# Kernel tuning notes

Measured on AMD Instinct MI355X. Metric: run time of the kernel, lower is better.

Reference implementation:

```python
import jax, jax.numpy as jnp
import numpy as np

DIM = 768
HEADS = 12
HEAD_DIM = DIM // HEADS  # 64
GRID = 48               # H = W = 48 tokens
RANK = 8                # LoRA rank


def setup_inputs() -> dict:
    key = jax.random.key(0)
    ks = jax.random.split(key, 20)
    s = 0.02
    inp = {
        "x": jax.random.normal(ks[0], (1, GRID, GRID, DIM), dtype=jnp.float32),
        "Wq": jax.random.normal(ks[1], (DIM, DIM), dtype=jnp.float32) * s,
        "bq": jax.random.normal(ks[2], (DIM,), dtype=jnp.float32) * s,
        "Wk": jax.random.normal(ks[3], (DIM, DIM), dtype=jnp.float32) * s,
        "bk": jax.random.normal(ks[4], (DIM,), dtype=jnp.float32) * s,
        "Wv": jax.random.normal(ks[5], (DIM, DIM), dtype=jnp.float32) * s,
        "bv": jax.random.normal(ks[6], (DIM,), dtype=jnp.float32) * s,
        "Wp": jax.random.normal(ks[7], (DIM, DIM), dtype=jnp.float32) * s,
        "bp": jax.random.normal(ks[8], (DIM,), dtype=jnp.float32) * s,
        "rel_pos_h": jax.random.normal(ks[9], (2 * GRID - 1, HEAD_DIM), dtype=jnp.float32) * s,
        "rel_pos_w": jax.random.normal(ks[10], (2 * GRID - 1, HEAD_DIM), dtype=jnp.float32) * s,
        "Aq": jax.random.normal(ks[11], (DIM, RANK), dtype=jnp.float32) * s,
        "Bq": jax.random.normal(ks[12], (RANK, DIM), dtype=jnp.float32) * s,
        "Ak": jax.random.normal(ks[13], (DIM, RANK), dtype=jnp.float32) * s,
        "Bk": jax.random.normal(ks[14], (RANK, DIM), dtype=jnp.float32) * s,
        "Av": jax.random.normal(ks[15], (DIM, RANK), dtype=jnp.float32) * s,
        "Bv": jax.random.normal(ks[16], (RANK, DIM), dtype=jnp.float32) * s,
    }
    return inp


def _get_rel_pos(size, rel_pos):
    # q_size == k_size == size, rel_pos has exactly 2*size-1 rows -> direct lookup
    idx = jnp.arange(size)[:, None] - jnp.arange(size)[None, :] + (size - 1)
    return rel_pos[idx]  # (size, size, head_dim)


def reference(x, Wq, bq, Wk, bk, Wv, bv, Wp, bp, rel_pos_h, rel_pos_w,
              Aq, Bq, Ak, Bk, Av, Bv):
    B, H, W, _ = x.shape
    N = H * W
    scale = HEAD_DIM ** -0.5

    # QKV projections + LoRA additions
    q = x @ Wq + bq + (x @ Aq) @ Bq
    k = x @ Wk + bk + (x @ Ak) @ Bk
    v = x @ Wv + bv + (x @ Av) @ Bv

    # (B, heads, N, head_dim)
    q = q.reshape(B, N, HEADS, HEAD_DIM).transpose(0, 2, 1, 3)
    k = k.reshape(B, N, HEADS, HEAD_DIM).transpose(0, 2, 1, 3)
    v = v.reshape(B, N, HEADS, HEAD_DIM).transpose(0, 2, 1, 3)

    attn = jnp.einsum('bhnc,bhmc->bhnm', q, k) * scale  # (B, heads, N, N)

    # Decomposed relative position bias (SAM add_decomposed_rel_pos)
    Rh = _get_rel_pos(H, rel_pos_h)  # (H, H, c)
    Rw = _get_rel_pos(W, rel_pos_w)  # (W, W, c)
    r_q = q.reshape(B, HEADS, H, W, HEAD_DIM)
    rel_h = jnp.einsum('bnhwc,hkc->bnhwk', r_q, Rh)  # (B, heads, H, W, H)
    rel_w = jnp.einsum('bnhwc,wkc->bnhwk', r_q, Rw)  # (B, heads, H, W, W)
    attn = (attn.reshape(B, HEADS, H, W, H, W)
            + rel_h[..., :, None] + rel_w[..., None, :]).reshape(B, HEADS, N, N)

    attn = jax.nn.softmax(attn, axis=-1)
    out = jnp.einsum('bhnm,bhmc->bhnc', attn, v)        # (B, heads, N, c)
    out = out.transpose(0, 2, 1, 3).reshape(B, H, W, DIM)
    return out @ Wp + bp
```

## Files before the change

kernel.cpp:

```cpp
#include <hip/hip_runtime.h>


#define DIM   768
#define HEADS 12
#define HD    64
#define NTOK  2304
#define RANK  8
#define GRD   48
#define CHUNKS 3
#define KEYS_PER_CHUNK 768
#define KT_PER 12
#define LOG2E 1.44269504088896f

typedef __attribute__((ext_vector_type(8))) short bf16x8;
typedef __attribute__((ext_vector_type(4))) float f32x4;
typedef unsigned short ushort_t;

__device__ __forceinline__ unsigned short f2bf(float x) {
    union { float f; unsigned u; } v; v.f = x;
    unsigned r = v.u + 0x7fffu + ((v.u >> 16) & 1u);
    return (unsigned short)(r >> 16);
}
__device__ __forceinline__ float bf2f(unsigned short h) {
    return __uint_as_float(((unsigned)h) << 16);
}
__device__ __forceinline__ void gload_lds16(const ushort_t* g, ushort_t* l) {
    __builtin_amdgcn_global_load_lds(
        (const __attribute__((address_space(1))) unsigned int*)g,
        (__attribute__((address_space(3))) unsigned int*)l, 16, 0, 0);
}

__global__ __launch_bounds__(256) void k_prep(
    const float* __restrict__ x, ushort_t* __restrict__ xb,
    const float* __restrict__ rph, const float* __restrict__ rpw,
    ushort_t* __restrict__ rphb, ushort_t* __restrict__ rpwb,
    const float* __restrict__ Wq, const float* __restrict__ Wk,
    const float* __restrict__ Wv, const float* __restrict__ Wp,
    const float* __restrict__ Aq, const float* __restrict__ Bq,
    const float* __restrict__ Ak, const float* __restrict__ Bk,
    const float* __restrict__ Av, const float* __restrict__ Bv,
    ushort_t* __restrict__ WT) {
    int bid = blockIdx.x, tid = threadIdx.x;

    if (bid < 1740) {
        if (bid < 1728) {
            int idx = (bid * 256 + tid) * 4;
            float4 v = *(const float4*)(x + idx);
            ushort4 o = make_ushort4(f2bf(v.x), f2bf(v.y), f2bf(v.z), f2bf(v.w));
            *(ushort4*)(xb + idx) = o;
        } else {
            int e = ((bid - 1728) * 256 + tid) * 4;
            const int TSZ = (2 * GRD - 1) * HD;
            if (e < TSZ) {
                float4 v = *(const float4*)(rph + e);
                ushort4 o = make_ushort4(f2bf(v.x), f2bf(v.y), f2bf(v.z), f2bf(v.w));
                *(ushort4*)(rphb + e) = o;
            } else if (e < 2 * TSZ) {
                float4 v = *(const float4*)(rpw + e - TSZ);
                ushort4 o = make_ushort4(f2bf(v.x), f2bf(v.y), f2bf(v.z), f2bf(v.w));
                *(ushort4*)(rpwb + e - TSZ) = o;
            }
        }
    }

    int kb = (bid % 24) * 32;
    int nb = (bid / 24) * 32;
    int sel = nb / DIM, nmod = nb % DIM;
    const float* W = (sel == 0) ? Wq : (sel == 1) ? Wk : (sel == 2) ? Wv : Wp;
    const float* A = (sel == 0) ? Aq : (sel == 1) ? Ak : Av;
    const float* B = (sel == 0) ? Bq : (sel == 1) ? Bk : Bv;
    __shared__ float T[32][33];
    for (int i = tid; i < 1024; i += 256) {
        int kl = i >> 5, nl = i & 31;
        float v = W[(kb + kl) * DIM + nmod + nl];
        if (sel < 3) {
            #pragma unroll
            for (int r = 0; r < RANK; r++)
                v += A[(kb + kl) * RANK + r] * B[r * DIM + nmod + nl];
        }
        T[kl][nl] = v;
    }
    __syncthreads();
    if (tid < 128) {
        int nl = tid >> 2, k8 = (tid & 3) * 8;
        ushort_t tmp[8];
        #pragma unroll
        for (int q = 0; q < 8; q++) tmp[q] = f2bf(T[k8 + q][nl]);
        *(uint4*)&WT[(size_t)(nb + nl) * DIM + kb + k8] = *(const uint4*)tmp;
    }
}

__global__ __launch_bounds__(256) void k_gemm_qkv(
    const ushort_t* __restrict__ xb, const ushort_t* __restrict__ WT,
    const float* __restrict__ bq, const float* __restrict__ bk,
    const float* __restrict__ bv,
    ushort_t* __restrict__ Qb, ushort_t* __restrict__ Kb,
    ushort_t* __restrict__ Vtb) {
    __shared__ __align__(16) ushort_t As[2][2][128 * 32];
    __shared__ __align__(16) ushort_t Bs[2][2][64 * 32];
    int tid = threadIdx.x;
    int wave = tid >> 6, lane = tid & 63, quad = lane >> 4, l16 = lane & 15;
    int wx = wave & 1, wy = wave >> 1;
    int nb = blockIdx.x * 64, mb = blockIdx.y * 128;

    f32x4 zero = {0.f, 0.f, 0.f, 0.f};
    f32x4 acc[4][2];
    #pragma unroll
    for (int i = 0; i < 4; i++)
        #pragma unroll
        for (int j = 0; j < 2; j++) acc[i][j] = zero;

    int rl = lane >> 2;
    int cl = (lane & 3) * 8;
    const ushort_t* gA = xb + (size_t)(mb + wave * 32 + rl) * DIM + cl;
    const ushort_t* gB = WT + (size_t)(nb + wave * 16 + rl) * DIM + cl;

    auto stage = [&](int k0, int b) {
        gload_lds16(gA + k0,                 &As[b][0][(wave * 32) * 32]);
        gload_lds16(gA + k0 + 16 * DIM,      &As[b][0][(wave * 32) * 32] + 16 * 32);
        gload_lds16(gA + k0 + 32,            &As[b][1][(wave * 32) * 32]);
        gload_lds16(gA + k0 + 32 + 16 * DIM, &As[b][1][(wave * 32) * 32] + 16 * 32);
        gload_lds16(gB + k0,                 &Bs[b][0][(wave * 16) * 32]);
        gload_lds16(gB + k0 + 32,            &Bs[b][1][(wave * 16) * 32]);
    };

    stage(0, 0);
    for (int it = 0; it < 12; ++it) {
        int cur = it & 1;
        if (it < 11) {
            stage((it + 1) * 64, cur ^ 1);
            asm volatile("s_waitcnt vmcnt(6)" ::: "memory");
        } else {
            asm volatile("s_waitcnt vmcnt(0)" ::: "memory");
        }
        __builtin_amdgcn_s_barrier();
        #pragma unroll
        for (int p = 0; p < 2; p++) {
            bf16x8 af[4], bf[2];
            #pragma unroll
            for (int i = 0; i < 4; i++)
                af[i] = *(const bf16x8*)&As[cur][p][(wy * 64 + i * 16 + l16) * 32 + quad * 8];
            #pragma unroll
            for (int j = 0; j < 2; j++)
                bf[j] = *(const bf16x8*)&Bs[cur][p][(wx * 32 + j * 16 + l16) * 32 + quad * 8];
            #pragma unroll
            for (int i = 0; i < 4; i++)
                #pragma unroll
                for (int j = 0; j < 2; j++)
                    acc[i][j] = __builtin_amdgcn_mfma_f32_16x16x32_bf16(af[i], bf[j], acc[i][j], 0, 0, 0);
        }
        __builtin_amdgcn_s_barrier();
    }

    ushort_t* pool = &As[0][0][0];
    int sel = nb / DIM;
    int rem0 = nb - sel * DIM;
    int hh = rem0 >> 6;
    const float* bias = (sel == 0) ? bq : (sel == 1) ? bk : bv;

    __syncthreads();

    if (sel < 2) {
        const int P = 72;
        #pragma unroll
        for (int j = 0; j < 2; j++) {
            int c = wx * 32 + j * 16 + l16;
            float bval = bias[rem0 + c];
            #pragma unroll
            for (int i = 0; i < 4; i++)
                #pragma unroll
                for (int r = 0; r < 4; r++) {
                    int row = wy * 64 + i * 16 + quad * 4 + r;
                    pool[row * P + c] = f2bf(acc[i][j][r] + bval);
                }
        }
        __syncthreads();
        ushort_t* qout = ((sel == 0) ? Qb : Kb) + (size_t)(hh * NTOK + mb) * HD;
        for (int idx = tid; idx < 128 * 8; idx += 256) {
            int row = idx >> 3, s8 = idx & 7;
            uint4 v = *(const uint4*)&pool[row * P + s8 * 8];
            *(uint4*)&qout[(size_t)row * HD + s8 * 8] = v;
        }
    } else {
        const int PV = 136;
        #pragma unroll
        for (int j = 0; j < 2; j++) {
            int c = wx * 32 + j * 16 + l16;
            float bval = bias[rem0 + c];
            #pragma unroll
            for (int i = 0; i < 4; i++)
                #pragma unroll
                for (int r = 0; r < 4; r++) {
                    int row = wy * 64 + i * 16 + quad * 4 + r;
                    pool[c * PV + row] = f2bf(acc[i][j][r] + bval);
                }
        }
        __syncthreads();
        ushort_t* vout = Vtb + (size_t)(hh * HD) * NTOK + mb;
        for (int idx = tid; idx < 64 * 16; idx += 256) {
            int cc = idx >> 4, r8 = idx & 15;
            uint4 v = *(const uint4*)&pool[cc * PV + r8 * 8];
            *(uint4*)&vout[(size_t)cc * NTOK + r8 * 8] = v;
        }
    }
}

__global__ __launch_bounds__(256) void k_relmm(
    const ushort_t* __restrict__ Qb, const ushort_t* __restrict__ rphb,
    const ushort_t* __restrict__ rpwb, float* __restrict__ relH,
    ushort_t* __restrict__ relWb) {
    int id = blockIdx.x * 4 + (threadIdx.x >> 6);
    int lane = threadIdx.x & 63, quad = lane >> 4, l16 = lane & 15;
    bool isW = id >= 1728;
    int t = isW ? id - 1728 : id;
    int ms = t % 3;
    int g  = (t / 3) % GRD;
    int h  = t / (3 * GRD);
    const ushort_t* tab = isW ? rpwb : rphb;

    f32x4 zero = {0.f, 0.f, 0.f, 0.f};
    f32x4 acc[3];
    #pragma unroll
    for (int ct = 0; ct < 3; ct++) acc[ct] = zero;

    bf16x8 bfr[3][2];
    #pragma unroll
    for (int ct = 0; ct < 3; ct++) {
        int trow = g + 47 - (ct * 16 + l16);
        bfr[ct][0] = *(const bf16x8*)&tab[(size_t)trow * HD + quad * 8];
        bfr[ct][1] = *(const bf16x8*)&tab[(size_t)trow * HD + 32 + quad * 8];
    }
    {
        int m = ms * 16 + l16;
        int n = isW ? m * GRD + g : g * GRD + m;
        bf16x8 a0 = *(const bf16x8*)&Qb[(size_t)(h * NTOK + n) * HD + quad * 8];
        bf16x8 a1 = *(const bf16x8*)&Qb[(size_t)(h * NTOK + n) * HD + 32 + quad * 8];
        #pragma unroll
        for (int ct = 0; ct < 3; ct++) {
            acc[ct] = __builtin_amdgcn_mfma_f32_16x16x32_bf16(a0, bfr[ct][0], acc[ct], 0, 0, 0);
            acc[ct] = __builtin_amdgcn_mfma_f32_16x16x32_bf16(a1, bfr[ct][1], acc[ct], 0, 0, 0);
        }
    }
    #pragma unroll
    for (int ct = 0; ct < 3; ct++) {
        #pragma unroll
        for (int r = 0; r < 4; r++) {
            int m = ms * 16 + quad * 4 + r;
            int n = isW ? m * GRD + g : g * GRD + m;
            int col = ct * 16 + l16;
            float val = acc[ct][r] * LOG2E;
            if (isW)
                relWb[(size_t)(h * NTOK + n) * GRD + col] = f2bf(val);
            else
                relH[(size_t)(h * NTOK + n) * GRD + col] = val;
        }
    }
}

__global__ __launch_bounds__(256, 3) void k_attn(
    const ushort_t* __restrict__ Qb, const ushort_t* __restrict__ Kb,
    const ushort_t* __restrict__ Vtb, const float* __restrict__ relH,
    const ushort_t* __restrict__ relWb, float* __restrict__ Opart,
    float* __restrict__ Lpart) {
    int h = blockIdx.x / CHUNKS, chunk = blockIdx.x - h * CHUNKS;
    int qt = blockIdx.y;
    int tid = threadIdx.x;
    int wave = tid >> 6, lane = tid & 63, quad = lane >> 4, l16 = lane & 15;
    int qbase = qt * 128;
    int kbase = chunk * KEYS_PER_CHUNK;

    __shared__ __align__(16) ushort_t Ks[64 * 68];
    __shared__ __align__(16) ushort_t Vs[64 * 68];
    __shared__ __align__(16) ushort_t Ps[4][32 * 68];
    __shared__ __align__(16) ushort_t rhs[128 * 18];

    for (int i = tid; i < 128 * 16; i += 256) {
        int r = i >> 4, c = i & 15;
        rhs[r * 18 + c] = f2bf(relH[(size_t)(h * NTOK + qbase + r) * GRD + chunk * 16 + c]);
    }

    bf16x8 qf[2][2];
    #pragma unroll
    for (int s = 0; s < 2; s++) {
        int qrow = qbase + wave * 32 + s * 16 + l16;
        qf[s][0] = *(const bf16x8*)&Qb[(size_t)(h * NTOK + qrow) * HD + quad * 8];
        qf[s][1] = *(const bf16x8*)&Qb[(size_t)(h * NTOK + qrow) * HD + 32 + quad * 8];
    }

    int r0 = tid >> 3, c0 = (tid & 7) * 8;
    const ushort_t* kg0 = Kb + (size_t)(h * NTOK + r0) * HD + c0;
    const ushort_t* kg1 = Kb + (size_t)(h * NTOK + r0 + 32) * HD + c0;
    const ushort_t* vg0 = Vtb + (size_t)(h * HD + r0) * NTOK + c0;
    const ushort_t* vg1 = Vtb + (size_t)(h * HD + r0 + 32) * NTOK + c0;
    int sk0 = r0 * 68 + c0, sk1 = sk0 + 32 * 68;

    const ushort_t* rw0 = relWb + (size_t)(h * NTOK + qbase + wave * 32 + l16) * GRD;
    const ushort_t* rw1 = rw0 + (size_t)16 * GRD;

    float lacc[2] = {0.f, 0.f};
    f32x4 zero = {0.f, 0.f, 0.f, 0.f};
    f32x4 oacc[2][4];
    #pragma unroll
    for (int s = 0; s < 2; s++)
        #pragma unroll
        for (int cs = 0; cs < 4; cs++) oacc[s][cs] = zero;

    const float scale2 = 0.125f * LOG2E;

    uint4 rk0 = *(const uint4*)(kg0 + (size_t)kbase * HD);
    uint4 rk1 = *(const uint4*)(kg1 + (size_t)kbase * HD);
    uint4 rv0 = *(const uint4*)(vg0 + kbase);
    uint4 rv1 = *(const uint4*)(vg1 + kbase);

    int kwS = quad * 4;
    int khlS = 0;

    for (int kt = 0; kt < KT_PER; kt++) {
        int kb = kbase + kt * 64;

        int kwA[4], khlA[4];
        kwA[0] = kwS; khlA[0] = khlS;
        #pragma unroll
        for (int ks = 1; ks < 4; ks++) {
            int kw = kwA[ks - 1] + 16, kh = khlA[ks - 1];
            if (kw >= 48) { kw -= 48; kh += 1; }
            kwA[ks] = kw; khlA[ks] = kh;
        }
        { int kw = kwA[3] + 16, kh = khlA[3];
          if (kw >= 48) { kw -= 48; kh += 1; }
          kwS = kw; khlS = kh; }

        __syncthreads();
        *(uint4*)&Ks[sk0] = rk0;  *(uint4*)&Ks[sk1] = rk1;
        *(uint4*)&Vs[sk0] = rv0;  *(uint4*)&Vs[sk1] = rv1;
        __syncthreads();

        uint2 rwv[2][4];
        #pragma unroll
        for (int ks = 0; ks < 4; ks++) {
            rwv[0][ks] = *(const uint2*)(rw0 + kwA[ks]);
            rwv[1][ks] = *(const uint2*)(rw1 + kwA[ks]);
        }

        if (kt < KT_PER - 1) {
            int kbn = kb + 64;
            rk0 = *(const uint4*)(kg0 + (size_t)kbn * HD);
            rk1 = *(const uint4*)(kg1 + (size_t)kbn * HD);
            rv0 = *(const uint4*)(vg0 + kbn);
            rv1 = *(const uint4*)(vg1 + kbn);
        }

        #pragma unroll
        for (int ks = 0; ks < 4; ks++) {
            bf16x8 kf0 = *(const bf16x8*)&Ks[(ks * 16 + l16) * 68 + quad * 8];
            bf16x8 kf1 = *(const bf16x8*)&Ks[(ks * 16 + l16) * 68 + 32 + quad * 8];
            f32x4 st[2];
            __builtin_amdgcn_s_setprio(1);
            #pragma unroll
            for (int s = 0; s < 2; s++) {
                f32x4 z = zero;
                z = __builtin_amdgcn_mfma_f32_16x16x32_bf16(kf0, qf[s][0], z, 0, 0, 0);
                z = __builtin_amdgcn_mfma_f32_16x16x32_bf16(kf1, qf[s][1], z, 0, 0, 0);
                st[s] = z;
            }
            __builtin_amdgcn_s_setprio(0);
            int khl = khlA[ks];
            #pragma unroll
            for (int s = 0; s < 2; s++) {
                int row = wave * 32 + s * 16 + l16;
                float rh = bf2f(rhs[row * 18 + khl]);
                uint2 u = rwv[s][ks];
                float p0 = __builtin_amdgcn_exp2f(st[s][0] * scale2 + rh + __uint_as_float(u.x << 16));
                float p1 = __builtin_amdgcn_exp2f(st[s][1] * scale2 + rh + __uint_as_float(u.x & 0xffff0000u));
                float p2 = __builtin_amdgcn_exp2f(st[s][2] * scale2 + rh + __uint_as_float(u.y << 16));
                float p3 = __builtin_amdgcn_exp2f(st[s][3] * scale2 + rh + __uint_as_float(u.y & 0xffff0000u));
                lacc[s] += (p0 + p1) + (p2 + p3);
                uint2 w;
                w.x = __builtin_amdgcn_perm(__float_as_uint(p1), __float_as_uint(p0), 0x07060302u);
                w.y = __builtin_amdgcn_perm(__float_as_uint(p3), __float_as_uint(p2), 0x07060302u);
                *(uint2*)&Ps[wave][(s * 16 + l16) * 68 + ks * 16 + quad * 4] = w;
            }
        }

        bf16x8 vf[4][2];
        #pragma unroll
        for (int cs = 0; cs < 4; cs++) {
            vf[cs][0] = *(const bf16x8*)&Vs[(cs * 16 + l16) * 68 + quad * 8];
            vf[cs][1] = *(const bf16x8*)&Vs[(cs * 16 + l16) * 68 + 32 + quad * 8];
        }
        __builtin_amdgcn_s_setprio(1);
        #pragma unroll
        for (int s = 0; s < 2; s++) {
            bf16x8 pa0 = *(const bf16x8*)&Ps[wave][(s * 16 + l16) * 68 + quad * 8];
            bf16x8 pa1 = *(const bf16x8*)&Ps[wave][(s * 16 + l16) * 68 + 32 + quad * 8];
            #pragma unroll
            for (int cs = 0; cs < 4; cs++) {
                oacc[s][cs] = __builtin_amdgcn_mfma_f32_16x16x32_bf16(pa0, vf[cs][0], oacc[s][cs], 0, 0, 0);
                oacc[s][cs] = __builtin_amdgcn_mfma_f32_16x16x32_bf16(pa1, vf[cs][1], oacc[s][cs], 0, 0, 0);
            }
        }
        __builtin_amdgcn_s_setprio(0);
    }

    #pragma unroll
    for (int s = 0; s < 2; s++) {
        float l = lacc[s];
        l += __shfl_xor(l, 16);
        l += __shfl_xor(l, 32);
        lacc[s] = l;
    }

    size_t obase = (size_t)(chunk * HEADS + h) * NTOK;
    #pragma unroll
    for (int s = 0; s < 2; s++) {
        #pragma unroll
        for (int cs = 0; cs < 4; cs++) {
            #pragma unroll
            for (int r = 0; r < 4; r++) {
                int row = qbase + wave * 32 + s * 16 + quad * 4 + r;
                Opart[(obase + row) * HD + cs * 16 + l16] = oacc[s][cs][r];
            }
        }
        if (quad == 0)
            Lpart[obase + qbase + wave * 32 + s * 16 + l16] = lacc[s];
    }
}

__global__ __launch_bounds__(256) void k_merge(const float* __restrict__ Opart,
                                               const float* __restrict__ Lpart,
                                               ushort_t* __restrict__ Ob) {
    int t = blockIdx.x * 256 + threadIdx.x;
    int e = t * 4;
    int c = e & (HD - 1);
    int row = (e >> 6) % NTOK;
    int h = e / (NTOK * HD);
    const int ostride = HEADS * NTOK * HD;
    float4 s = {0.f, 0.f, 0.f, 0.f};
    float l = 0.f;
    #pragma unroll
    for (int ch = 0; ch < CHUNKS; ch++) {
        float4 v = *(const float4*)&Opart[(size_t)ch * ostride + e];
        s.x += v.x; s.y += v.y; s.z += v.z; s.w += v.w;
        l += Lpart[(size_t)(ch * HEADS + h) * NTOK + row];
    }
    float inv = 1.0f / l;
    ushort4 o = make_ushort4(f2bf(s.x * inv), f2bf(s.y * inv),
                             f2bf(s.z * inv), f2bf(s.w * inv));
    *(ushort4*)&Ob[(size_t)row * DIM + h * HD + c] = o;
}

__global__ __launch_bounds__(256) void k_gemm_proj(
    const ushort_t* __restrict__ Ob, const ushort_t* __restrict__ WTp,
    const float* __restrict__ bp, float* __restrict__ out) {
    __shared__ __align__(16) ushort_t As[2][2][64 * 32];
    __shared__ __align__(16) ushort_t Bs[2][2][64 * 32];
    int tid = threadIdx.x;
    int wave = tid >> 6, lane = tid & 63, quad = lane >> 4, l16 = lane & 15;
    int wx = wave & 1, wy = wave >> 1;
    int nb = blockIdx.x * 64, mb = blockIdx.y * 64;

    f32x4 zero = {0.f, 0.f, 0.f, 0.f};
    f32x4 acc[2][2];
    #pragma unroll
    for (int i = 0; i < 2; i++)
        #pragma unroll
        for (int j = 0; j < 2; j++) acc[i][j] = zero;

    int rl = lane >> 2;
    int cl = (lane & 3) * 8;
    const ushort_t* gA = Ob + (size_t)(mb + wave * 16 + rl) * DIM + cl;
    const ushort_t* gB = WTp + (size_t)(nb + wave * 16 + rl) * DIM + cl;

    auto stage = [&](int k0, int b) {
        gload_lds16(gA + k0,      &As[b][0][(wave * 16) * 32]);
        gload_lds16(gA + k0 + 32, &As[b][1][(wave * 16) * 32]);
        gload_lds16(gB + k0,      &Bs[b][0][(wave * 16) * 32]);
        gload_lds16(gB + k0 + 32, &Bs[b][1][(wave * 16) * 32]);
    };

    stage(0, 0);
    for (int it = 0; it < 12; ++it) {
        int cur = it & 1;
        if (it < 11) {
            stage((it + 1) * 64, cur ^ 1);
            asm volatile("s_waitcnt vmcnt(4)" ::: "memory");
        } else {
            asm volatile("s_waitcnt vmcnt(0)" ::: "memory");
        }
        __builtin_amdgcn_s_barrier();
        #pragma unroll
        for (int p = 0; p < 2; p++) {
            bf16x8 af[2], bf[2];
            #pragma unroll
            for (int i = 0; i < 2; i++)
                af[i] = *(const bf16x8*)&As[cur][p][(wy * 32 + i * 16 + l16) * 32 + quad * 8];
            #pragma unroll
            for (int j = 0; j < 2; j++)
                bf[j] = *(const bf16x8*)&Bs[cur][p][(wx * 32 + j * 16 + l16) * 32 + quad * 8];
            #pragma unroll
            for (int i = 0; i < 2; i++)
                #pragma unroll
                for (int j = 0; j < 2; j++)
                    acc[i][j] = __builtin_amdgcn_mfma_f32_16x16x32_bf16(af[i], bf[j], acc[i][j], 0, 0, 0);
        }
        __builtin_amdgcn_s_barrier();
    }

    #pragma unroll
    for (int j = 0; j < 2; j++) {
        int col = nb + wx * 32 + j * 16 + l16;
        float bval = bp[col];
        #pragma unroll
        for (int i = 0; i < 2; i++) {
            #pragma unroll
            for (int r = 0; r < 4; r++) {
                int row = mb + wy * 32 + i * 16 + quad * 4 + r;
                out[(size_t)row * DIM + col] = acc[i][j][r] + bval;
            }
        }
    }
}

extern "C" void kernel_launch(void* const* d_in, const int* in_sizes, int n_in,
                              void* d_out, int out_size, void* d_ws, size_t ws_size,
                              hipStream_t stream) {
    const float* x   = (const float*)d_in[0];
    const float* Wq  = (const float*)d_in[1];
    const float* bq  = (const float*)d_in[2];
    const float* Wk  = (const float*)d_in[3];
    const float* bk  = (const float*)d_in[4];
    const float* Wv  = (const float*)d_in[5];
    const float* bv  = (const float*)d_in[6];
    const float* Wp  = (const float*)d_in[7];
    const float* bp  = (const float*)d_in[8];
    const float* rph = (const float*)d_in[9];
    const float* rpw = (const float*)d_in[10];
    const float* Aq  = (const float*)d_in[11];
    const float* Bq  = (const float*)d_in[12];
    const float* Ak  = (const float*)d_in[13];
    const float* Bk  = (const float*)d_in[14];
    const float* Av  = (const float*)d_in[15];
    const float* Bv  = (const float*)d_in[16];
    float* out = (float*)d_out;

    char* w = (char*)d_ws;
    size_t off = 0;
    auto carve = [&](size_t bytes) {
        char* p = w + off;
        off += (bytes + 255) & ~(size_t)255;
        return p;
    };
    ushort_t* xb    = (ushort_t*)carve((size_t)NTOK * DIM * 2);
    ushort_t* WT    = (ushort_t*)carve((size_t)4 * DIM * DIM * 2);
    ushort_t* Qb    = (ushort_t*)carve((size_t)HEADS * NTOK * HD * 2);
    ushort_t* Kb    = (ushort_t*)carve((size_t)HEADS * NTOK * HD * 2);
    ushort_t* Vtb   = (ushort_t*)carve((size_t)HEADS * HD * NTOK * 2);
    float*    relH  = (float*)carve((size_t)HEADS * NTOK * GRD * 4);
    ushort_t* relWb = (ushort_t*)carve((size_t)HEADS * NTOK * GRD * 2);
    ushort_t* Ob    = (ushort_t*)carve((size_t)NTOK * DIM * 2);
    float*    Opart = (float*)carve((size_t)CHUNKS * HEADS * NTOK * HD * 4);
    float*    Lpart = (float*)carve((size_t)CHUNKS * HEADS * NTOK * 4);
    ushort_t* rphb  = (ushort_t*)carve((size_t)(2 * GRD - 1) * HD * 2);
    ushort_t* rpwb  = (ushort_t*)carve((size_t)(2 * GRD - 1) * HD * 2);

    k_prep<<<dim3(2304), dim3(256), 0, stream>>>(
        x, xb, rph, rpw, rphb, rpwb,
        Wq, Wk, Wv, Wp, Aq, Bq, Ak, Bk, Av, Bv, WT);
    k_gemm_qkv<<<dim3(36, 18), dim3(256), 0, stream>>>(
        xb, WT, bq, bk, bv, Qb, Kb, Vtb);
    k_relmm<<<dim3(864), dim3(256), 0, stream>>>(
        Qb, rphb, rpwb, relH, relWb);
    k_attn<<<dim3(HEADS * CHUNKS, NTOK / 128), dim3(256), 0, stream>>>(
        Qb, Kb, Vtb, relH, relWb, Opart, Lpart);
    k_merge<<<dim3(HEADS * NTOK * HD / (256 * 4)), dim3(256), 0, stream>>>(
        Opart, Lpart, Ob);
    k_gemm_proj<<<dim3(12, 36), dim3(256), 0, stream>>>(
        Ob, WT + (size_t)3 * DIM * DIM, bp, out);
}
```

Measured before the change: 173.9 us.

## Fuse split-K attention merge into attention kernel via last-block atomic counter

Removes the separate merge kernel launch. Each attention block writes its partial output and log-sum, then bumps a per-(head, query tile) atomic counter, and the last of the three chunk blocks reduces the partials and writes the bf16 output. This saves one kernel launch and its scheduling gap. In exchange it adds thread fences, an atomic per block, and a serialized merge tail in the last block. The counters are reset in the prep kernel.

New measurement: 311.3 us. 79.0% more time.

```diff
diff --git a/kernel.cpp b/kernel.cpp
--- a/kernel.cpp
+++ b/kernel.cpp
@@ -10,6 +10,7 @@
 #define CHUNKS 3
 #define KEYS_PER_CHUNK 768
 #define KT_PER 12
+#define QTILES 18
 #define LOG2E 1.44269504088896f
 
 typedef __attribute__((ext_vector_type(8))) short bf16x8;
@@ -39,8 +40,10 @@
     const float* __restrict__ Aq, const float* __restrict__ Bq,
     const float* __restrict__ Ak, const float* __restrict__ Bk,
     const float* __restrict__ Av, const float* __restrict__ Bv,
-    ushort_t* __restrict__ WT) {
+    ushort_t* __restrict__ WT, int* __restrict__ cnt) {
     int bid = blockIdx.x, tid = threadIdx.x;
+
+    if (bid == 0 && tid < HEADS * QTILES) cnt[tid] = 0;
 
     if (bid < 1740) {
         if (bid < 1728) {
@@ -261,7 +264,8 @@
     const ushort_t* __restrict__ Qb, const ushort_t* __restrict__ Kb,
     const ushort_t* __restrict__ Vtb, const float* __restrict__ relH,
     const ushort_t* __restrict__ relWb, float* __restrict__ Opart,
-    float* __restrict__ Lpart) {
+    float* __restrict__ Lpart, ushort_t* __restrict__ Ob,
+    int* __restrict__ cnt) {
     int h = blockIdx.x / CHUNKS, chunk = blockIdx.x - h * CHUNKS;
     int qt = blockIdx.y;
     int tid = threadIdx.x;
@@ -273,6 +277,7 @@
     __shared__ __align__(16) ushort_t Vs[64 * 68];
     __shared__ __align__(16) ushort_t Ps[4][32 * 68];
     __shared__ __align__(16) ushort_t rhs[128 * 18];
+    __shared__ int lastFlag;
 
     for (int i = tid; i < 128 * 16; i += 256) {
         int r = i >> 4, c = i & 15;
@@ -424,29 +429,35 @@
         if (quad == 0)
             Lpart[obase + qbase + wave * 32 + s * 16 + l16] = lacc[s];
     }
-}
-
-__global__ __launch_bounds__(256) void k_merge(const float* __restrict__ Opart,
-                                               const float* __restrict__ Lpart,
-                                               ushort_t* __restrict__ Ob) {
-    int t = blockIdx.x * 256 + threadIdx.x;
-    int e = t * 4;
-    int c = e & (HD - 1);
-    int row = (e >> 6) % NTOK;
-    int h = e / (NTOK * HD);
-    const int ostride = HEADS * NTOK * HD;
-    float4 s = {0.f, 0.f, 0.f, 0.f};
-    float l = 0.f;
-    #pragma unroll
-    for (int ch = 0; ch < CHUNKS; ch++) {
-        float4 v = *(const float4*)&Opart[(size_t)ch * ostride + e];
-        s.x += v.x; s.y += v.y; s.z += v.z; s.w += v.w;
-        l += Lpart[(size_t)(ch * HEADS + h) * NTOK + row];
-    }
-    float inv = 1.0f / l;
-    ushort4 o = make_ushort4(f2bf(s.x * inv), f2bf(s.y * inv),
-                             f2bf(s.z * inv), f2bf(s.w * inv));
-    *(ushort4*)&Ob[(size_t)row * DIM + h * HD + c] = o;
+
+    __threadfence();
+    __syncthreads();
+    if (tid == 0) {
+        int prev = atomicAdd(&cnt[h * QTILES + qt], 1);
+        lastFlag = (prev == CHUNKS - 1);
+    }
+    __syncthreads();
+    if (lastFlag) {
+        __threadfence();
+        const int ostride = HEADS * NTOK * HD;
+        for (int idx = tid; idx < 128 * 16; idx += 256) {
+            int row = idx >> 4, cg = (idx & 15) * 4;
+            int grow = qbase + row;
+            size_t e = ((size_t)h * NTOK + grow) * HD + cg;
+            float4 s4 = {0.f, 0.f, 0.f, 0.f};
+            float l = 0.f;
+            #pragma unroll
+            for (int ch = 0; ch < CHUNKS; ch++) {
+                float4 v = *(const float4*)&Opart[(size_t)ch * ostride + e];
+                s4.x += v.x; s4.y += v.y; s4.z += v.z; s4.w += v.w;
+                l += Lpart[(size_t)(ch * HEADS + h) * NTOK + grow];
+            }
+            float inv = 1.0f / l;
+            ushort4 o = make_ushort4(f2bf(s4.x * inv), f2bf(s4.y * inv),
+                                     f2bf(s4.z * inv), f2bf(s4.w * inv));
+            *(ushort4*)&Ob[(size_t)grow * DIM + h * HD + cg] = o;
+        }
+    }
 }
 
 __global__ __launch_bounds__(256) void k_gemm_proj(
@@ -562,18 +573,17 @@
     float*    Lpart = (float*)carve((size_t)CHUNKS * HEADS * NTOK * 4);
     ushort_t* rphb  = (ushort_t*)carve((size_t)(2 * GRD - 1) * HD * 2);
     ushort_t* rpwb  = (ushort_t*)carve((size_t)(2 * GRD - 1) * HD * 2);
+    int*      cnt   = (int*)carve((size_t)HEADS * QTILES * 4);
 
     k_prep<<<dim3(2304), dim3(256), 0, stream>>>(
         x, xb, rph, rpw, rphb, rpwb,
-        Wq, Wk, Wv, Wp, Aq, Bq, Ak, Bk, Av, Bv, WT);
+        Wq, Wk, Wv, Wp, Aq, Bq, Ak, Bk, Av, Bv, WT, cnt);
     k_gemm_qkv<<<dim3(36, 18), dim3(256), 0, stream>>>(
         xb, WT, bq, bk, bv, Qb, Kb, Vtb);
     k_relmm<<<dim3(864), dim3(256), 0, stream>>>(
         Qb, rphb, rpwb, relH, relWb);
     k_attn<<<dim3(HEADS * CHUNKS, NTOK / 128), dim3(256), 0, stream>>>(
-        Qb, Kb, Vtb, relH, relWb, Opart, Lpart);
-    k_merge<<<dim3(HEADS * NTOK * HD / (256 * 4)), dim3(256), 0, stream>>>(
-        Opart, Lpart, Ob);
+        Qb, Kb, Vtb, relH, relWb, Opart, Lpart, Ob, cnt);
     k_gemm_proj<<<dim3(12, 36), dim3(256), 0, stream>>>(
         Ob, WT + (size_t)3 * DIM * DIM, bp, out);
 }
```
